# Kernel tuning notes

Hardware: AMD Instinct MI355X
Metric: run time of the kernel (lower is better)

Reference implementation:

```python
import jax, jax.numpy as jnp
import numpy as np

B, C, D_BB, D = 16384, 4, 2048, 512
MAX_NORM = 3.0
LN_EPS = 1e-5


def setup_inputs() -> dict:
    key = jax.random.key(0)
    ks = jax.random.split(key, 6)
    return {
        "thumbnails": jax.random.normal(ks[0], (B, C, D_BB), dtype=jnp.float32),
        # nn.Linear(backbone_dim, hidden_dim): weight [D, D_BB], bias [D]
        "proj_w": jax.random.normal(ks[1], (D, D_BB), dtype=jnp.float32) / np.float32(np.sqrt(D_BB)),
        "proj_b": jnp.zeros((D,), dtype=jnp.float32),
        # per-camera LayerNorm affine params [C, D]
        "gamma": jnp.ones((C, D), dtype=jnp.float32),
        "beta": jnp.zeros((C, D), dtype=jnp.float32),
        # per-camera SwiGLU weights (no bias), torch Linear convention [out, in]
        "w_gate": jax.random.normal(ks[2], (C, D, D), dtype=jnp.float32) / np.float32(np.sqrt(D)),
        "w_val": jax.random.normal(ks[3], (C, D, D), dtype=jnp.float32) / np.float32(np.sqrt(D)),
        # per-camera output proj D->36 (zero-init in module; small random for a useful baseline)
        "w_out": jax.random.normal(ks[4], (C, 36, D), dtype=jnp.float32) * np.float32(0.02),
    }


def _expm66(A):
    """Matrix exponential of [..., 6, 6] matrices with ||A||_F <= MAX_NORM.

    Scaling-and-squaring with a fixed order-12 Taylor series. After scaling by
    2^-4, ||A/16|| <= 0.1875, so the order-12 truncation error is << fp32 eps.
    Matches torch.linalg.matrix_exp to fp32 precision and is fully transposable.
    """
    s = 4  # number of squarings
    As = A * jnp.asarray(1.0 / (2 ** s), A.dtype)
    I = jnp.broadcast_to(jnp.eye(6, dtype=A.dtype), A.shape)
    E = I
    term = I
    for k in range(1, 13):
        term = jnp.matmul(term, As) * jnp.asarray(1.0 / k, A.dtype)
        E = E + term
    for _ in range(s):
        E = jnp.matmul(E, E)
    return E


def reference(thumbnails, proj_w, proj_b, gamma, beta, w_gate, w_val, w_out):
    # thumbnail projection: [B,C,D_BB] @ [D,D_BB]^T -> [B,C,D]
    reg = jnp.einsum('bce,de->bcd', thumbnails, proj_w) + proj_b
    # per-camera LayerNorm (biased variance, as in torch)
    mu = jnp.mean(reg, axis=-1, keepdims=True)
    var = jnp.var(reg, axis=-1, keepdims=True)
    xn = (reg - mu) * jax.lax.rsqrt(var + LN_EPS) * gamma + beta  # gamma/beta broadcast [C,D]
    # SwiGLU (per-camera weights)
    gate = jnp.einsum('bcd,cfd->bcf', xn, w_gate)
    val = jnp.einsum('bcd,cfd->bcf', xn, w_val)
    h = jax.nn.silu(gate) * val
    # project to Lie algebra, skew-symmetrize
    A = jnp.einsum('bcf,cof->bco', h, w_out).reshape(B, C, 6, 6)
    A = A - jnp.swapaxes(A, -1, -2)
    # Frobenius-norm clip to MAX_NORM
    frob = jnp.sqrt(jnp.sum(A * A, axis=(-2, -1), keepdims=True))
    A = A * (jnp.minimum(frob, MAX_NORM) / jnp.maximum(frob, 1e-8))
    # matrix exponential -> orthogonal deltaM, returned as [C, B, 6, 6]
    dM = _expm66(A)
    return jnp.swapaxes(dM, 0, 1)
```

## Files before the change

### kernel.cpp

```cpp
#include <hip/hip_runtime.h>
#include <cstdint>
#include <cstddef>


#define B_SZ   16384
#define C_CAM  4
#define DBB    2048
#define D_H    512

typedef __attribute__((ext_vector_type(8))) short  bf16x8;
typedef __attribute__((ext_vector_type(4))) float  f32x4;

__device__ __forceinline__ unsigned short f2b(float f) {
    union { float f; unsigned u; } v; v.f = f;
    unsigned r = (v.u + 0x7FFFu + ((v.u >> 16) & 1u)) >> 16;
    return (unsigned short)r;
}
__device__ __forceinline__ float b2f(unsigned short u) {
    union { unsigned u; float f; } v; v.u = ((unsigned)u) << 16;
    return v.f;
}

#define GLDS(g, l) __builtin_amdgcn_global_load_lds( \
    (const __attribute__((address_space(1))) unsigned int*)(g), \
    (__attribute__((address_space(3))) unsigned int*)(l), 16, 0, 0)

__global__ void k_cvt(const float* __restrict__ src, unsigned short* __restrict__ dst, int n) {
    int i = blockIdx.x * blockDim.x + threadIdx.x;
    int stride = gridDim.x * blockDim.x;
    for (; i < n; i += stride) dst[i] = f2b(src[i]);
}

__global__ __launch_bounds__(256)
void k_cvt8(const float* __restrict__ src, unsigned short* __restrict__ dst, long n8) {
    long i = (long)blockIdx.x * blockDim.x + threadIdx.x;
    if (i >= n8) return;
    const float4 a = ((const float4*)src)[i * 2];
    const float4 b = ((const float4*)src)[i * 2 + 1];
    unsigned short o[8] = {f2b(a.x), f2b(a.y), f2b(a.z), f2b(a.w),
                           f2b(b.x), f2b(b.y), f2b(b.z), f2b(b.w)};
    ((uint4*)dst)[i] = *(const uint4*)o;
}

__global__ void k_cvt_wout(const float* __restrict__ src, unsigned short* __restrict__ dst) {
    int i = blockIdx.x * blockDim.x + threadIdx.x;
    if (i >= C_CAM * 48 * D_H) return;
    int col = i & (D_H - 1);
    int row = (i >> 9) % 48;
    int c   = i / (48 * D_H);
    dst[i] = (row < 36) ? f2b(src[((size_t)c * 36 + row) * D_H + col]) : (unsigned short)0;
}

__global__ __launch_bounds__(256)
void k_projb(const unsigned short* __restrict__ A, const unsigned short* __restrict__ Bw,
             const float* __restrict__ bias, unsigned short* __restrict__ regb) {
    __shared__ unsigned short lsA[128 * 32];
    __shared__ unsigned short lsB[128 * 32];
    const int t = threadIdx.x;
    const int tile_n = blockIdx.x * 128;
    const int tile_m = blockIdx.y * 128;
    const int w = t >> 6, l = t & 63, lr = l & 15, quad = l >> 4;
    const int wm = (w >> 1) * 64, wn = (w & 1) * 64;

    f32x4 acc[4][4];
#pragma unroll
    for (int i = 0; i < 4; i++)
#pragma unroll
        for (int j = 0; j < 4; j++) acc[i][j] = (f32x4){0.f, 0.f, 0.f, 0.f};

    const int srow = l >> 2, scol = (l & 3) * 8;
    const unsigned short* baseA = A  + (size_t)(tile_m + w * 32 + srow) * DBB + scol;
    const unsigned short* baseB = Bw + (size_t)(tile_n + w * 32 + srow) * DBB + scol;
    unsigned short* ldsAw = &lsA[w * 32 * 32];
    unsigned short* ldsBw = &lsB[w * 32 * 32];

    for (int kt = 0; kt < DBB / 32; ++kt) {
        __syncthreads();
        GLDS(baseA + kt * 32,            ldsAw);
        GLDS(baseA + kt * 32 + 16 * DBB, ldsAw + 16 * 32);
        GLDS(baseB + kt * 32,            ldsBw);
        GLDS(baseB + kt * 32 + 16 * DBB, ldsBw + 16 * 32);
        __syncthreads();
        bf16x8 af[4], bfr[4];
#pragma unroll
        for (int i = 0; i < 4; i++)
            af[i] = *(const bf16x8*)(&lsA[(wm + i * 16 + lr) * 32 + quad * 8]);
#pragma unroll
        for (int j = 0; j < 4; j++)
            bfr[j] = *(const bf16x8*)(&lsB[(wn + j * 16 + lr) * 32 + quad * 8]);
#pragma unroll
        for (int i = 0; i < 4; i++)
#pragma unroll
            for (int j = 0; j < 4; j++)
                acc[i][j] = __builtin_amdgcn_mfma_f32_16x16x32_bf16(af[i], bfr[j], acc[i][j], 0, 0, 0);
    }
#pragma unroll
    for (int j = 0; j < 4; j++) {
        const int col = tile_n + wn + j * 16 + lr;
        const float bv = bias[col];
#pragma unroll
        for (int i = 0; i < 4; i++)
#pragma unroll
            for (int r = 0; r < 4; r++) {
                const int row = tile_m + wm + i * 16 + quad * 4 + r;
                regb[(size_t)row * D_H + col] = f2b(acc[i][j][r] + bv);
            }
    }
}

__global__ __launch_bounds__(256)
void k_projf(const float* __restrict__ A, const unsigned short* __restrict__ Bw,
             const float* __restrict__ bias, unsigned short* __restrict__ regb) {
    __shared__ unsigned short lsA[128 * 72];
    __shared__ unsigned short lsB[128 * 72];
    const int t = threadIdx.x;
    const int tile_n = blockIdx.x * 128;
    const int tile_m = blockIdx.y * 128;
    const int w = t >> 6, l = t & 63, lr = l & 15, quad = l >> 4;
    const int wm = (w >> 1) * 64, wn = (w & 1) * 64;

    f32x4 acc[4][4];
#pragma unroll
    for (int i = 0; i < 4; i++)
#pragma unroll
        for (int j = 0; j < 4; j++) acc[i][j] = (f32x4){0.f, 0.f, 0.f, 0.f};

    const int ar = t >> 4, ac = (t & 15) * 4;
    const int br = t >> 3, bc = (t & 7) * 8;

    for (int kt = 0; kt < DBB / 64; ++kt) {
        __syncthreads();
#pragma unroll
        for (int p = 0; p < 8; p++) {
            const int row = p * 16 + ar;
            const float4 v = *(const float4*)(A + (size_t)(tile_m + row) * DBB + kt * 64 + ac);
            unsigned p0 = (unsigned)f2b(v.x) | ((unsigned)f2b(v.y) << 16);
            unsigned p1 = (unsigned)f2b(v.z) | ((unsigned)f2b(v.w) << 16);
            *(uint2*)(&lsA[row * 72 + ac]) = make_uint2(p0, p1);
        }
#pragma unroll
        for (int p = 0; p < 4; p++) {
            const int row = p * 32 + br;
            *(uint4*)(&lsB[row * 72 + bc]) =
                *(const uint4*)(Bw + (size_t)(tile_n + row) * DBB + kt * 64 + bc);
        }
        __syncthreads();
#pragma unroll
        for (int kk = 0; kk < 2; ++kk) {
            bf16x8 af[4], bfr[4];
#pragma unroll
            for (int i = 0; i < 4; i++)
                af[i] = *(const bf16x8*)(&lsA[(wm + i * 16 + lr) * 72 + kk * 32 + quad * 8]);
#pragma unroll
            for (int j = 0; j < 4; j++)
                bfr[j] = *(const bf16x8*)(&lsB[(wn + j * 16 + lr) * 72 + kk * 32 + quad * 8]);
#pragma unroll
            for (int i = 0; i < 4; i++)
#pragma unroll
                for (int j = 0; j < 4; j++)
                    acc[i][j] = __builtin_amdgcn_mfma_f32_16x16x32_bf16(af[i], bfr[j], acc[i][j], 0, 0, 0);
        }
    }
#pragma unroll
    for (int j = 0; j < 4; j++) {
        const int col = tile_n + wn + j * 16 + lr;
        const float bv = bias[col];
#pragma unroll
        for (int i = 0; i < 4; i++)
#pragma unroll
            for (int r = 0; r < 4; r++) {
                const int row = tile_m + wm + i * 16 + quad * 4 + r;
                regb[(size_t)row * D_H + col] = f2b(acc[i][j][r] + bv);
            }
    }
}

__global__ __launch_bounds__(256)
void k_ln(const unsigned short* __restrict__ regb, const float* __restrict__ gamma,
          const float* __restrict__ beta, unsigned short* __restrict__ xnb) {
    const int t = threadIdx.x;
    const int wave = t >> 6, l = t & 63;
    const int r = blockIdx.x * 4 + wave;
    const int c = r & 3, b = r >> 2;

    const uint4 pk = *(const uint4*)(regb + (size_t)r * D_H + l * 8);
    const unsigned short* ps = (const unsigned short*)&pk;
    float x[8];
#pragma unroll
    for (int j = 0; j < 8; j++) x[j] = b2f(ps[j]);

    float s = 0.f, ss = 0.f;
#pragma unroll
    for (int j = 0; j < 8; j++) { s += x[j]; ss += x[j] * x[j]; }
#pragma unroll
    for (int off = 32; off > 0; off >>= 1) {
        s  += __shfl_xor(s, off);
        ss += __shfl_xor(ss, off);
    }
    const float mu  = s * (1.0f / 512.0f);
    const float var = ss * (1.0f / 512.0f) - mu * mu;
    const float rs  = rsqrtf(var + 1e-5f);

    unsigned short o[8];
#pragma unroll
    for (int j = 0; j < 8; j++) {
        const int d = l * 8 + j;
        o[j] = f2b((x[j] - mu) * rs * gamma[c * D_H + d] + beta[c * D_H + d]);
    }
    *(uint4*)(xnb + ((size_t)c * B_SZ + b) * D_H + l * 8) = *(const uint4*)o;
}

__global__ __launch_bounds__(256)
void k_swiglu(const unsigned short* __restrict__ xnb, const unsigned short* __restrict__ wg,
              const unsigned short* __restrict__ wv, unsigned short* __restrict__ hb) {
    __shared__ unsigned short lsA[128 * 32];
    __shared__ unsigned short lsG[128 * 32];
    __shared__ unsigned short lsV[128 * 32];
    const int t = threadIdx.x;
    const int tile_n = blockIdx.x * 128;
    const int tile_m = blockIdx.y * 128;
    const int cam = blockIdx.z;
    const unsigned short* Ac = xnb + (size_t)cam * B_SZ * D_H;
    const unsigned short* Gc = wg + (size_t)cam * D_H * D_H;
    const unsigned short* Vc = wv + (size_t)cam * D_H * D_H;
    const int w = t >> 6, l = t & 63, lr = l & 15, quad = l >> 4;
    const int wm = (w >> 1) * 64, wn = (w & 1) * 64;

    f32x4 ag[4][4], av[4][4];
#pragma unroll
    for (int i = 0; i < 4; i++)
#pragma unroll
        for (int j = 0; j < 4; j++) { ag[i][j] = (f32x4){0.f,0.f,0.f,0.f}; av[i][j] = (f32x4){0.f,0.f,0.f,0.f}; }

    const int srow = l >> 2, scol = (l & 3) * 8;
    const unsigned short* baseA = Ac + (size_t)(tile_m + w * 32 + srow) * D_H + scol;
    const unsigned short* baseG = Gc + (size_t)(tile_n + w * 32 + srow) * D_H + scol;
    const unsigned short* baseV = Vc + (size_t)(tile_n + w * 32 + srow) * D_H + scol;
    unsigned short* ldsAw = &lsA[w * 32 * 32];
    unsigned short* ldsGw = &lsG[w * 32 * 32];
    unsigned short* ldsVw = &lsV[w * 32 * 32];

    for (int kt = 0; kt < D_H / 32; ++kt) {
        __syncthreads();
        GLDS(baseA + kt * 32,            ldsAw);
        GLDS(baseA + kt * 32 + 16 * D_H, ldsAw + 16 * 32);
        GLDS(baseG + kt * 32,            ldsGw);
        GLDS(baseG + kt * 32 + 16 * D_H, ldsGw + 16 * 32);
        GLDS(baseV + kt * 32,            ldsVw);
        GLDS(baseV + kt * 32 + 16 * D_H, ldsVw + 16 * 32);
        __syncthreads();
        bf16x8 af[4];
#pragma unroll
        for (int i = 0; i < 4; i++)
            af[i] = *(const bf16x8*)(&lsA[(wm + i * 16 + lr) * 32 + quad * 8]);
#pragma unroll
        for (int j = 0; j < 4; j++) {
            bf16x8 gf = *(const bf16x8*)(&lsG[(wn + j * 16 + lr) * 32 + quad * 8]);
            bf16x8 vf = *(const bf16x8*)(&lsV[(wn + j * 16 + lr) * 32 + quad * 8]);
#pragma unroll
            for (int i = 0; i < 4; i++) {
                ag[i][j] = __builtin_amdgcn_mfma_f32_16x16x32_bf16(af[i], gf, ag[i][j], 0, 0, 0);
                av[i][j] = __builtin_amdgcn_mfma_f32_16x16x32_bf16(af[i], vf, av[i][j], 0, 0, 0);
            }
        }
    }
#pragma unroll
    for (int i = 0; i < 4; i++)
#pragma unroll
        for (int j = 0; j < 4; j++)
#pragma unroll
            for (int r = 0; r < 4; r++) {
                const int row = tile_m + wm + i * 16 + quad * 4 + r;
                const int col = tile_n + wn + j * 16 + lr;
                const float g = ag[i][j][r], v = av[i][j][r];
                const float h = g * v / (1.0f + __expf(-g));
                hb[((size_t)cam * B_SZ + row) * D_H + col] = f2b(h);
            }
}

__global__ __launch_bounds__(256)
void k_outproj(const unsigned short* __restrict__ hb, const unsigned short* __restrict__ wo,
               float* __restrict__ Abuf) {
    __shared__ unsigned short lsA[128 * 32];
    __shared__ unsigned short lsB[48 * 32];
    const int t = threadIdx.x;
    const int tile_m = blockIdx.y * 128;
    const int cam = blockIdx.z;
    const unsigned short* Ac = hb + (size_t)cam * B_SZ * D_H;
    const unsigned short* Bc = wo + (size_t)cam * 48 * D_H;
    const int w = t >> 6, l = t & 63, lr = l & 15, quad = l >> 4;
    const int srow = l >> 2, scol = (l & 3) * 8;

    f32x4 acc[2][3];
#pragma unroll
    for (int i = 0; i < 2; i++)
#pragma unroll
        for (int j = 0; j < 3; j++) acc[i][j] = (f32x4){0.f,0.f,0.f,0.f};

    const unsigned short* baseA = Ac + (size_t)(tile_m + w * 32 + srow) * D_H + scol;
    const unsigned short* baseB = Bc + (size_t)(w * 16 + srow) * D_H + scol;
    unsigned short* ldsAw = &lsA[w * 32 * 32];
    unsigned short* ldsBw = &lsB[w * 16 * 32];

    for (int kt = 0; kt < D_H / 32; ++kt) {
        __syncthreads();
        GLDS(baseA + kt * 32,            ldsAw);
        GLDS(baseA + kt * 32 + 16 * D_H, ldsAw + 16 * 32);
        if (w < 3) GLDS(baseB + kt * 32, ldsBw);
        __syncthreads();
        bf16x8 af[2], bfr[3];
#pragma unroll
        for (int i = 0; i < 2; i++)
            af[i] = *(const bf16x8*)(&lsA[(w * 32 + i * 16 + lr) * 32 + quad * 8]);
#pragma unroll
        for (int j = 0; j < 3; j++)
            bfr[j] = *(const bf16x8*)(&lsB[(j * 16 + lr) * 32 + quad * 8]);
#pragma unroll
        for (int i = 0; i < 2; i++)
#pragma unroll
            for (int j = 0; j < 3; j++)
                acc[i][j] = __builtin_amdgcn_mfma_f32_16x16x32_bf16(af[i], bfr[j], acc[i][j], 0, 0, 0);
    }
#pragma unroll
    for (int i = 0; i < 2; i++)
#pragma unroll
        for (int j = 0; j < 3; j++)
#pragma unroll
            for (int r = 0; r < 4; r++) {
                const int col = j * 16 + lr;
                if (col < 36) {
                    const int row = tile_m + w * 32 + i * 16 + quad * 4 + r;
                    Abuf[((size_t)cam * B_SZ + row) * 36 + col] = acc[i][j][r];
                }
            }
}

__global__ __launch_bounds__(128)
void k_expm(const float* __restrict__ Abuf, float* __restrict__ out) {
    const int gid = blockIdx.x * blockDim.x + threadIdx.x;
    if (gid >= B_SZ * C_CAM) return;
    const float* Ap = Abuf + (size_t)gid * 36;

    float a[36];
#pragma unroll
    for (int i = 0; i < 36; i++) a[i] = Ap[i];

    float S[36];
#pragma unroll
    for (int i = 0; i < 6; i++)
#pragma unroll
        for (int j = 0; j < 6; j++) S[i * 6 + j] = a[i * 6 + j] - a[j * 6 + i];

    float fr2 = 0.f;
#pragma unroll
    for (int i = 0; i < 36; i++) fr2 += S[i] * S[i];
    const float fr = sqrtf(fr2);
    const float sc = fminf(fr, 3.0f) / fmaxf(fr, 1e-8f) * 0.0625f;

    float As[36];
#pragma unroll
    for (int i = 0; i < 36; i++) As[i] = S[i] * sc;

    float E[36], T[36], tmp[36];
#pragma unroll
    for (int i = 0; i < 36; i++) { E[i] = (i % 7 == 0) ? 1.f : 0.f; T[i] = E[i]; }

#pragma unroll
    for (int k = 1; k <= 12; k++) {
        const float invk = 1.0f / (float)k;
#pragma unroll
        for (int i = 0; i < 6; i++)
#pragma unroll
            for (int j = 0; j < 6; j++) {
                float sum = 0.f;
#pragma unroll
                for (int q = 0; q < 6; q++) sum += T[i * 6 + q] * As[q * 6 + j];
                tmp[i * 6 + j] = sum * invk;
            }
#pragma unroll
        for (int i = 0; i < 36; i++) { T[i] = tmp[i]; E[i] += tmp[i]; }
    }
#pragma unroll
    for (int sq = 0; sq < 4; sq++) {
#pragma unroll
        for (int i = 0; i < 6; i++)
#pragma unroll
            for (int j = 0; j < 6; j++) {
                float sum = 0.f;
#pragma unroll
                for (int q = 0; q < 6; q++) sum += E[i * 6 + q] * E[q * 6 + j];
                tmp[i * 6 + j] = sum;
            }
#pragma unroll
        for (int i = 0; i < 36; i++) E[i] = tmp[i];
    }

    float* op = out + (size_t)gid * 36;
#pragma unroll
    for (int i = 0; i < 36; i++) op[i] = E[i];
}

extern "C" void kernel_launch(void* const* d_in, const int* in_sizes, int n_in,
                              void* d_out, int out_size, void* d_ws, size_t ws_size,
                              hipStream_t stream) {
    const float* thumb  = (const float*)d_in[0];
    const float* proj_w = (const float*)d_in[1];
    const float* proj_b = (const float*)d_in[2];
    const float* gamma  = (const float*)d_in[3];
    const float* beta   = (const float*)d_in[4];
    const float* w_gate = (const float*)d_in[5];
    const float* w_val  = (const float*)d_in[6];
    const float* w_out  = (const float*)d_in[7];

    char* ws = (char*)d_ws;
    const size_t FAST_WS = 409141248ULL;

    if (ws_size >= FAST_WS) {
        unsigned short* Abf  = (unsigned short*)(ws);
        unsigned short* regb = (unsigned short*)(ws + 268435456);
        unsigned short* xnb  = (unsigned short*)(ws + 335544320);
        unsigned short* hb   = (unsigned short*)(ws);
        float*          Abuf = (float*)(ws + 268435456);
        unsigned short* pwb  = (unsigned short*)(ws + 402653184);
        unsigned short* wgb  = (unsigned short*)(ws + 404750336);
        unsigned short* wvb  = (unsigned short*)(ws + 406847488);
        unsigned short* wob  = (unsigned short*)(ws + 408944640);

        hipLaunchKernelGGL(k_cvt8, dim3(65536), dim3(256), 0, stream,
                           thumb, Abf, (long)B_SZ * C_CAM * DBB / 8);
        hipLaunchKernelGGL(k_cvt, dim3(1024), dim3(256), 0, stream, proj_w, pwb, D_H * DBB);
        hipLaunchKernelGGL(k_cvt, dim3(1024), dim3(256), 0, stream, w_gate, wgb, C_CAM * D_H * D_H);
        hipLaunchKernelGGL(k_cvt, dim3(1024), dim3(256), 0, stream, w_val, wvb, C_CAM * D_H * D_H);
        hipLaunchKernelGGL(k_cvt_wout, dim3((C_CAM * 48 * D_H + 255) / 256), dim3(256), 0, stream, w_out, wob);

        hipLaunchKernelGGL(k_projb, dim3(4, 512), dim3(256), 0, stream, Abf, pwb, proj_b, regb);
        hipLaunchKernelGGL(k_ln, dim3(B_SZ * C_CAM / 4), dim3(256), 0, stream, regb, gamma, beta, xnb);
        hipLaunchKernelGGL(k_swiglu, dim3(4, 128, 4), dim3(256), 0, stream, xnb, wgb, wvb, hb);
        hipLaunchKernelGGL(k_outproj, dim3(1, 128, 4), dim3(256), 0, stream, hb, wob, Abuf);
        hipLaunchKernelGGL(k_expm, dim3(B_SZ * C_CAM / 128), dim3(128), 0, stream, Abuf, (float*)d_out);
    } else {
        unsigned short* regb = (unsigned short*)(ws + 0);
        unsigned short* xnb  = (unsigned short*)(ws + 67108864);
        unsigned short* hb   = (unsigned short*)(ws + 0);
        float*          Abuf = (float*)(ws + 67108864);
        unsigned short* pwb  = (unsigned short*)(ws + 134217728);
        unsigned short* wgb  = (unsigned short*)(ws + 136314880);
        unsigned short* wvb  = (unsigned short*)(ws + 138412032);
        unsigned short* wob  = (unsigned short*)(ws + 140509184);

        hipLaunchKernelGGL(k_cvt, dim3(1024), dim3(256), 0, stream, proj_w, pwb, D_H * DBB);
        hipLaunchKernelGGL(k_cvt, dim3(1024), dim3(256), 0, stream, w_gate, wgb, C_CAM * D_H * D_H);
        hipLaunchKernelGGL(k_cvt, dim3(1024), dim3(256), 0, stream, w_val, wvb, C_CAM * D_H * D_H);
        hipLaunchKernelGGL(k_cvt_wout, dim3((C_CAM * 48 * D_H + 255) / 256), dim3(256), 0, stream, w_out, wob);

        hipLaunchKernelGGL(k_projf, dim3(4, 512), dim3(256), 0, stream, thumb, pwb, proj_b, regb);
        hipLaunchKernelGGL(k_ln, dim3(B_SZ * C_CAM / 4), dim3(256), 0, stream, regb, gamma, beta, xnb);
        hipLaunchKernelGGL(k_swiglu, dim3(4, 128, 4), dim3(256), 0, stream, xnb, wgb, wvb, hb);
        hipLaunchKernelGGL(k_outproj, dim3(1, 128, 4), dim3(256), 0, stream, hb, wob, Abuf);
        hipLaunchKernelGGL(k_expm, dim3(B_SZ * C_CAM / 128), dim3(128), 0, stream, Abuf, (float*)d_out);
    }
}
```

Measured before the change: 1.183 ms.

## Fuse fp32-to-bf16 conversion, projection GEMM and LayerNorm into one kernel

Replaces the separate thumbnail bf16 conversion pass, the projection GEMM and the LayerNorm kernel with a single 512-thread kernel. Each block computes a full 128x512 output row tile, so LayerNorm statistics can be reduced in registers and shared memory. The kernel converts fp32 thumbnails to bf16 on the fly with a one-step register prefetch, and writes normalized bf16 output directly in camera-major layout. This removes the 268MB bf16 copy of the input and the intermediate regb round trip. In exchange it uses larger per-thread accumulators (128 floats), which may cut occupancy, and the synchronous A-tile staging may expose load latency.

```diff
diff --git a/kernel.cpp b/kernel.cpp
--- a/kernel.cpp
+++ b/kernel.cpp
@@ -29,17 +29,6 @@
     int i = blockIdx.x * blockDim.x + threadIdx.x;
     int stride = gridDim.x * blockDim.x;
     for (; i < n; i += stride) dst[i] = f2b(src[i]);
-}
-
-__global__ __launch_bounds__(256)
-void k_cvt8(const float* __restrict__ src, unsigned short* __restrict__ dst, long n8) {
-    long i = (long)blockIdx.x * blockDim.x + threadIdx.x;
-    if (i >= n8) return;
-    const float4 a = ((const float4*)src)[i * 2];
-    const float4 b = ((const float4*)src)[i * 2 + 1];
-    unsigned short o[8] = {f2b(a.x), f2b(a.y), f2b(a.z), f2b(a.w),
-                           f2b(b.x), f2b(b.y), f2b(b.z), f2b(b.w)};
-    ((uint4*)dst)[i] = *(const uint4*)o;
 }
 
 __global__ void k_cvt_wout(const float* __restrict__ src, unsigned short* __restrict__ dst) {
@@ -51,163 +40,143 @@
     dst[i] = (row < 36) ? f2b(src[((size_t)c * 36 + row) * D_H + col]) : (unsigned short)0;
 }
 
-__global__ __launch_bounds__(256)
-void k_projb(const unsigned short* __restrict__ A, const unsigned short* __restrict__ Bw,
-             const float* __restrict__ bias, unsigned short* __restrict__ regb) {
+__global__ __launch_bounds__(512)
+void k_projln(const float* __restrict__ A, const unsigned short* __restrict__ Bw,
+              const float* __restrict__ bias, const float* __restrict__ gamma,
+              const float* __restrict__ beta, unsigned short* __restrict__ xnb) {
     __shared__ unsigned short lsA[128 * 32];
-    __shared__ unsigned short lsB[128 * 32];
+    __shared__ unsigned short lsB[512 * 32];
+    __shared__ float red[2][128][4];
+
     const int t = threadIdx.x;
-    const int tile_n = blockIdx.x * 128;
-    const int tile_m = blockIdx.y * 128;
+    const int tile_m = blockIdx.x * 128;
     const int w = t >> 6, l = t & 63, lr = l & 15, quad = l >> 4;
-    const int wm = (w >> 1) * 64, wn = (w & 1) * 64;
-
-    f32x4 acc[4][4];
+    const int wm = (w >> 2) * 64;
+    const int wn = (w & 3) * 128;
+
+    f32x4 acc[4][8];
 #pragma unroll
     for (int i = 0; i < 4; i++)
 #pragma unroll
-        for (int j = 0; j < 4; j++) acc[i][j] = (f32x4){0.f, 0.f, 0.f, 0.f};
+        for (int j = 0; j < 8; j++) acc[i][j] = (f32x4){0.f, 0.f, 0.f, 0.f};
+
+    const int arow = t >> 2, acol = (t & 3) * 8;
+    const float* baseA = A + (size_t)(tile_m + arow) * DBB + acol;
+    unsigned short* ldsAdst = &lsA[arow * 32 + acol];
 
     const int srow = l >> 2, scol = (l & 3) * 8;
-    const unsigned short* baseA = A  + (size_t)(tile_m + w * 32 + srow) * DBB + scol;
-    const unsigned short* baseB = Bw + (size_t)(tile_n + w * 32 + srow) * DBB + scol;
-    unsigned short* ldsAw = &lsA[w * 32 * 32];
-    unsigned short* ldsBw = &lsB[w * 32 * 32];
+    const unsigned short* baseB = Bw + (size_t)(w * 64 + srow) * DBB + scol;
+    unsigned short* ldsBw = &lsB[w * 64 * 32];
+
+    float4 pa0 = *(const float4*)(baseA);
+    float4 pa1 = *(const float4*)(baseA + 4);
 
     for (int kt = 0; kt < DBB / 32; ++kt) {
         __syncthreads();
-        GLDS(baseA + kt * 32,            ldsAw);
-        GLDS(baseA + kt * 32 + 16 * DBB, ldsAw + 16 * 32);
+        {
+            unsigned short o[8] = {f2b(pa0.x), f2b(pa0.y), f2b(pa0.z), f2b(pa0.w),
+                                   f2b(pa1.x), f2b(pa1.y), f2b(pa1.z), f2b(pa1.w)};
+            *(uint4*)ldsAdst = *(const uint4*)o;
+        }
         GLDS(baseB + kt * 32,            ldsBw);
         GLDS(baseB + kt * 32 + 16 * DBB, ldsBw + 16 * 32);
-        __syncthreads();
-        bf16x8 af[4], bfr[4];
+        GLDS(baseB + kt * 32 + 32 * DBB, ldsBw + 32 * 32);
+        GLDS(baseB + kt * 32 + 48 * DBB, ldsBw + 48 * 32);
+        __syncthreads();
+
+        bf16x8 af[4];
 #pragma unroll
         for (int i = 0; i < 4; i++)
             af[i] = *(const bf16x8*)(&lsA[(wm + i * 16 + lr) * 32 + quad * 8]);
-#pragma unroll
-        for (int j = 0; j < 4; j++)
-            bfr[j] = *(const bf16x8*)(&lsB[(wn + j * 16 + lr) * 32 + quad * 8]);
+
+        if (kt < DBB / 32 - 1) {
+            pa0 = *(const float4*)(baseA + (kt + 1) * 32);
+            pa1 = *(const float4*)(baseA + (kt + 1) * 32 + 4);
+        }
+
+#pragma unroll
+        for (int j = 0; j < 8; j++) {
+            const bf16x8 bfr = *(const bf16x8*)(&lsB[(wn + j * 16 + lr) * 32 + quad * 8]);
+#pragma unroll
+            for (int i = 0; i < 4; i++)
+                acc[i][j] = __builtin_amdgcn_mfma_f32_16x16x32_bf16(af[i], bfr, acc[i][j], 0, 0, 0);
+        }
+    }
+
+#pragma unroll
+    for (int j = 0; j < 8; j++) {
+        const float bv = bias[wn + j * 16 + lr];
 #pragma unroll
         for (int i = 0; i < 4; i++)
 #pragma unroll
-            for (int j = 0; j < 4; j++)
-                acc[i][j] = __builtin_amdgcn_mfma_f32_16x16x32_bf16(af[i], bfr[j], acc[i][j], 0, 0, 0);
-    }
-#pragma unroll
-    for (int j = 0; j < 4; j++) {
-        const int col = tile_n + wn + j * 16 + lr;
-        const float bv = bias[col];
+            for (int r = 0; r < 4; r++) acc[i][j][r] += bv;
+    }
+
+    float s[4][4], ss[4][4];
+#pragma unroll
+    for (int i = 0; i < 4; i++)
+#pragma unroll
+        for (int r = 0; r < 4; r++) {
+            float a = 0.f, b = 0.f;
+#pragma unroll
+            for (int j = 0; j < 8; j++) { const float x = acc[i][j][r]; a += x; b += x * x; }
+            s[i][r] = a; ss[i][r] = b;
+        }
+#pragma unroll
+    for (int off = 1; off <= 8; off <<= 1) {
 #pragma unroll
         for (int i = 0; i < 4; i++)
 #pragma unroll
             for (int r = 0; r < 4; r++) {
-                const int row = tile_m + wm + i * 16 + quad * 4 + r;
-                regb[(size_t)row * D_H + col] = f2b(acc[i][j][r] + bv);
-            }
-    }
-}
-
-__global__ __launch_bounds__(256)
-void k_projf(const float* __restrict__ A, const unsigned short* __restrict__ Bw,
-             const float* __restrict__ bias, unsigned short* __restrict__ regb) {
-    __shared__ unsigned short lsA[128 * 72];
-    __shared__ unsigned short lsB[128 * 72];
-    const int t = threadIdx.x;
-    const int tile_n = blockIdx.x * 128;
-    const int tile_m = blockIdx.y * 128;
-    const int w = t >> 6, l = t & 63, lr = l & 15, quad = l >> 4;
-    const int wm = (w >> 1) * 64, wn = (w & 1) * 64;
-
-    f32x4 acc[4][4];
+                s[i][r]  += __shfl_xor(s[i][r], off);
+                ss[i][r] += __shfl_xor(ss[i][r], off);
+            }
+    }
+    if (lr == 0) {
+#pragma unroll
+        for (int i = 0; i < 4; i++)
+#pragma unroll
+            for (int r = 0; r < 4; r++) {
+                const int rloc = wm + i * 16 + quad * 4 + r;
+                red[0][rloc][w & 3] = s[i][r];
+                red[1][rloc][w & 3] = ss[i][r];
+            }
+    }
+    __syncthreads();
+
+    float mu[4][4], rs[4][4];
 #pragma unroll
     for (int i = 0; i < 4; i++)
 #pragma unroll
-        for (int j = 0; j < 4; j++) acc[i][j] = (f32x4){0.f, 0.f, 0.f, 0.f};
-
-    const int ar = t >> 4, ac = (t & 15) * 4;
-    const int br = t >> 3, bc = (t & 7) * 8;
-
-    for (int kt = 0; kt < DBB / 64; ++kt) {
-        __syncthreads();
-#pragma unroll
-        for (int p = 0; p < 8; p++) {
-            const int row = p * 16 + ar;
-            const float4 v = *(const float4*)(A + (size_t)(tile_m + row) * DBB + kt * 64 + ac);
-            unsigned p0 = (unsigned)f2b(v.x) | ((unsigned)f2b(v.y) << 16);
-            unsigned p1 = (unsigned)f2b(v.z) | ((unsigned)f2b(v.w) << 16);
-            *(uint2*)(&lsA[row * 72 + ac]) = make_uint2(p0, p1);
-        }
-#pragma unroll
-        for (int p = 0; p < 4; p++) {
-            const int row = p * 32 + br;
-            *(uint4*)(&lsB[row * 72 + bc]) =
-                *(const uint4*)(Bw + (size_t)(tile_n + row) * DBB + kt * 64 + bc);
-        }
-        __syncthreads();
-#pragma unroll
-        for (int kk = 0; kk < 2; ++kk) {
-            bf16x8 af[4], bfr[4];
-#pragma unroll
-            for (int i = 0; i < 4; i++)
-                af[i] = *(const bf16x8*)(&lsA[(wm + i * 16 + lr) * 72 + kk * 32 + quad * 8]);
-#pragma unroll
-            for (int j = 0; j < 4; j++)
-                bfr[j] = *(const bf16x8*)(&lsB[(wn + j * 16 + lr) * 72 + kk * 32 + quad * 8]);
-#pragma unroll
-            for (int i = 0; i < 4; i++)
-#pragma unroll
-                for (int j = 0; j < 4; j++)
-                    acc[i][j] = __builtin_amdgcn_mfma_f32_16x16x32_bf16(af[i], bfr[j], acc[i][j], 0, 0, 0);
-        }
-    }
-#pragma unroll
-    for (int j = 0; j < 4; j++) {
-        const int col = tile_n + wn + j * 16 + lr;
-        const float bv = bias[col];
-#pragma unroll
-        for (int i = 0; i < 4; i++)
+        for (int r = 0; r < 4; r++) {
+            const int rloc = wm + i * 16 + quad * 4 + r;
+            const float S  = red[0][rloc][0] + red[0][rloc][1] + red[0][rloc][2] + red[0][rloc][3];
+            const float SS = red[1][rloc][0] + red[1][rloc][1] + red[1][rloc][2] + red[1][rloc][3];
+            const float m_ = S * (1.0f / 512.0f);
+            const float v_ = SS * (1.0f / 512.0f) - m_ * m_;
+            mu[i][r] = m_;
+            rs[i][r] = rsqrtf(v_ + 1e-5f);
+        }
+
+#pragma unroll
+    for (int j = 0; j < 8; j++) {
+        const int col = wn + j * 16 + lr;
+        float gv[4], bt[4];
+#pragma unroll
+        for (int r = 0; r < 4; r++) {
+            gv[r] = gamma[r * D_H + col];
+            bt[r] = beta[r * D_H + col];
+        }
+#pragma unroll
+        for (int i = 0; i < 4; i++) {
+            const int bidx = (tile_m + wm + i * 16 + quad * 4) >> 2;
 #pragma unroll
             for (int r = 0; r < 4; r++) {
-                const int row = tile_m + wm + i * 16 + quad * 4 + r;
-                regb[(size_t)row * D_H + col] = f2b(acc[i][j][r] + bv);
-            }
-    }
-}
-
-__global__ __launch_bounds__(256)
-void k_ln(const unsigned short* __restrict__ regb, const float* __restrict__ gamma,
-          const float* __restrict__ beta, unsigned short* __restrict__ xnb) {
-    const int t = threadIdx.x;
-    const int wave = t >> 6, l = t & 63;
-    const int r = blockIdx.x * 4 + wave;
-    const int c = r & 3, b = r >> 2;
-
-    const uint4 pk = *(const uint4*)(regb + (size_t)r * D_H + l * 8);
-    const unsigned short* ps = (const unsigned short*)&pk;
-    float x[8];
-#pragma unroll
-    for (int j = 0; j < 8; j++) x[j] = b2f(ps[j]);
-
-    float s = 0.f, ss = 0.f;
-#pragma unroll
-    for (int j = 0; j < 8; j++) { s += x[j]; ss += x[j] * x[j]; }
-#pragma unroll
-    for (int off = 32; off > 0; off >>= 1) {
-        s  += __shfl_xor(s, off);
-        ss += __shfl_xor(ss, off);
-    }
-    const float mu  = s * (1.0f / 512.0f);
-    const float var = ss * (1.0f / 512.0f) - mu * mu;
-    const float rs  = rsqrtf(var + 1e-5f);
-
-    unsigned short o[8];
-#pragma unroll
-    for (int j = 0; j < 8; j++) {
-        const int d = l * 8 + j;
-        o[j] = f2b((x[j] - mu) * rs * gamma[c * D_H + d] + beta[c * D_H + d]);
-    }
-    *(uint4*)(xnb + ((size_t)c * B_SZ + b) * D_H + l * 8) = *(const uint4*)o;
+                const float x = (acc[i][j][r] - mu[i][r]) * rs[i][r] * gv[r] + bt[r];
+                xnb[((size_t)r * B_SZ + bidx) * D_H + col] = f2b(x);
+            }
+        }
+    }
 }
 
 __global__ __launch_bounds__(256)
@@ -413,50 +382,22 @@
     const float* w_out  = (const float*)d_in[7];
 
     char* ws = (char*)d_ws;
-    const size_t FAST_WS = 409141248ULL;
-
-    if (ws_size >= FAST_WS) {
-        unsigned short* Abf  = (unsigned short*)(ws);
-        unsigned short* regb = (unsigned short*)(ws + 268435456);
-        unsigned short* xnb  = (unsigned short*)(ws + 335544320);
-        unsigned short* hb   = (unsigned short*)(ws);
-        float*          Abuf = (float*)(ws + 268435456);
-        unsigned short* pwb  = (unsigned short*)(ws + 402653184);
-        unsigned short* wgb  = (unsigned short*)(ws + 404750336);
-        unsigned short* wvb  = (unsigned short*)(ws + 406847488);
-        unsigned short* wob  = (unsigned short*)(ws + 408944640);
-
-        hipLaunchKernelGGL(k_cvt8, dim3(65536), dim3(256), 0, stream,
-                           thumb, Abf, (long)B_SZ * C_CAM * DBB / 8);
-        hipLaunchKernelGGL(k_cvt, dim3(1024), dim3(256), 0, stream, proj_w, pwb, D_H * DBB);
-        hipLaunchKernelGGL(k_cvt, dim3(1024), dim3(256), 0, stream, w_gate, wgb, C_CAM * D_H * D_H);
-        hipLaunchKernelGGL(k_cvt, dim3(1024), dim3(256), 0, stream, w_val, wvb, C_CAM * D_H * D_H);
-        hipLaunchKernelGGL(k_cvt_wout, dim3((C_CAM * 48 * D_H + 255) / 256), dim3(256), 0, stream, w_out, wob);
-
-        hipLaunchKernelGGL(k_projb, dim3(4, 512), dim3(256), 0, stream, Abf, pwb, proj_b, regb);
-        hipLaunchKernelGGL(k_ln, dim3(B_SZ * C_CAM / 4), dim3(256), 0, stream, regb, gamma, beta, xnb);
-        hipLaunchKernelGGL(k_swiglu, dim3(4, 128, 4), dim3(256), 0, stream, xnb, wgb, wvb, hb);
-        hipLaunchKernelGGL(k_outproj, dim3(1, 128, 4), dim3(256), 0, stream, hb, wob, Abuf);
-        hipLaunchKernelGGL(k_expm, dim3(B_SZ * C_CAM / 128), dim3(128), 0, stream, Abuf, (float*)d_out);
-    } else {
-        unsigned short* regb = (unsigned short*)(ws + 0);
-        unsigned short* xnb  = (unsigned short*)(ws + 67108864);
-        unsigned short* hb   = (unsigned short*)(ws + 0);
-        float*          Abuf = (float*)(ws + 67108864);
-        unsigned short* pwb  = (unsigned short*)(ws + 134217728);
-        unsigned short* wgb  = (unsigned short*)(ws + 136314880);
-        unsigned short* wvb  = (unsigned short*)(ws + 138412032);
-        unsigned short* wob  = (unsigned short*)(ws + 140509184);
-
-        hipLaunchKernelGGL(k_cvt, dim3(1024), dim3(256), 0, stream, proj_w, pwb, D_H * DBB);
-        hipLaunchKernelGGL(k_cvt, dim3(1024), dim3(256), 0, stream, w_gate, wgb, C_CAM * D_H * D_H);
-        hipLaunchKernelGGL(k_cvt, dim3(1024), dim3(256), 0, stream, w_val, wvb, C_CAM * D_H * D_H);
-        hipLaunchKernelGGL(k_cvt_wout, dim3((C_CAM * 48 * D_H + 255) / 256), dim3(256), 0, stream, w_out, wob);
-
-        hipLaunchKernelGGL(k_projf, dim3(4, 512), dim3(256), 0, stream, thumb, pwb, proj_b, regb);
-        hipLaunchKernelGGL(k_ln, dim3(B_SZ * C_CAM / 4), dim3(256), 0, stream, regb, gamma, beta, xnb);
-        hipLaunchKernelGGL(k_swiglu, dim3(4, 128, 4), dim3(256), 0, stream, xnb, wgb, wvb, hb);
-        hipLaunchKernelGGL(k_outproj, dim3(1, 128, 4), dim3(256), 0, stream, hb, wob, Abuf);
-        hipLaunchKernelGGL(k_expm, dim3(B_SZ * C_CAM / 128), dim3(128), 0, stream, Abuf, (float*)d_out);
-    }
-}
+    unsigned short* xnb  = (unsigned short*)(ws);
+    float*          Abuf = (float*)(ws);
+    unsigned short* hb   = (unsigned short*)(ws + 67108864);
+    unsigned short* pwb  = (unsigned short*)(ws + 134217728);
+    unsigned short* wgb  = (unsigned short*)(ws + 136314880);
+    unsigned short* wvb  = (unsigned short*)(ws + 138412032);
+    unsigned short* wob  = (unsigned short*)(ws + 140509184);
+
+    hipLaunchKernelGGL(k_cvt, dim3(1024), dim3(256), 0, stream, proj_w, pwb, D_H * DBB);
+    hipLaunchKernelGGL(k_cvt, dim3(1024), dim3(256), 0, stream, w_gate, wgb, C_CAM * D_H * D_H);
+    hipLaunchKernelGGL(k_cvt, dim3(1024), dim3(256), 0, stream, w_val, wvb, C_CAM * D_H * D_H);
+    hipLaunchKernelGGL(k_cvt_wout, dim3((C_CAM * 48 * D_H + 255) / 256), dim3(256), 0, stream, w_out, wob);
+
+    hipLaunchKernelGGL(k_projln, dim3(B_SZ * C_CAM / 128), dim3(512), 0, stream,
+                       thumb, pwb, proj_b, gamma, beta, xnb);
+    hipLaunchKernelGGL(k_swiglu, dim3(4, 128, 4), dim3(256), 0, stream, xnb, wgb, wvb, hb);
+    hipLaunchKernelGGL(k_outproj, dim3(1, 128, 4), dim3(256), 0, stream, hb, wob, Abuf);
+    hipLaunchKernelGGL(k_expm, dim3(B_SZ * C_CAM / 128), dim3(128), 0, stream, Abuf, (float*)d_out);
+}
```

New measurement: 1.080 ms. -8.7%, faster.
